# Performance work log

Hardware: AMD Instinct MI355X
Metric: run time of the kernel (lower is better)

## Reference

```python
import jax, jax.numpy as jnp
import numpy as np
from jax import lax

B, C, H, W = 8, 128, 128, 128


def setup_inputs() -> dict:
    key = jax.random.key(0)
    ks = jax.random.split(key, 10)
    s = 0.02
    return {
        "x": jax.random.normal(ks[0], (B, C, H, W), jnp.float32),
        "ln_w": jnp.ones((C,), jnp.float32),
        "ln_b": jnp.zeros((C,), jnp.float32),
        "qkv_w": jax.random.normal(ks[1], (3 * C, C, 1, 1), jnp.float32) * s,
        "qkv_b": jnp.zeros((3 * C,), jnp.float32),
        "dw_w": jax.random.normal(ks[2], (3 * C, 1, 3, 3), jnp.float32) * s,
        "dw_b": jnp.zeros((3 * C,), jnp.float32),
        "proj_w": jax.random.normal(ks[3], (C, C, 1, 1), jnp.float32) * s,
        "proj_b": jnp.zeros((C,), jnp.float32),
        "temp1": jnp.ones((1, 1), jnp.float32),
        "temp2": jnp.ones((1, 1), jnp.float32),
    }


def reference(x, ln_w, ln_b, qkv_w, qkv_b, dw_w, dw_b, proj_w, proj_b, temp1, temp2):
    Cd = x.shape[1]

    def ln(t):  # WithBias LayerNorm over channel dim (unbiased=False var)
        mu = t.mean(axis=1, keepdims=True)
        var = ((t - mu) ** 2).mean(axis=1, keepdims=True)
        return (t - mu) / jnp.sqrt(var + 1e-5) * ln_w[None, :, None, None] + ln_b[None, :, None, None]

    def conv1(t, w, b):  # 1x1 conv
        return jnp.einsum('bchw,oc->bohw', t, w[:, :, 0, 0]) + b[None, :, None, None]

    def dwc(t):  # depthwise 3x3, pad 1
        y = lax.conv_general_dilated(t, dw_w, (1, 1), ((1, 1), (1, 1)),
                                     dimension_numbers=('NCHW', 'OIHW', 'NCHW'),
                                     feature_group_count=t.shape[1])
        return y + dw_b[None, :, None, None]

    def l2n(t):  # F.normalize over last axis, eps=1e-12
        return t / jnp.maximum(jnp.linalg.norm(t, axis=-1, keepdims=True), 1e-12)

    # ---- stage 1: pool over H, attention over W (channel-pooled) ----
    qkv = dwc(conv1(ln(x), qkv_w, qkv_b))
    q1, k1, v1 = qkv[:, :Cd], qkv[:, Cd:2 * Cd], qkv[:, 2 * Cd:]
    q1 = l2n(q1.mean(axis=2)[:, None])           # [B,1,C,W]
    k1 = l2n(k1.max(axis=2)[:, None])            # [B,1,C,W]
    attn1 = jax.nn.softmax(jnp.einsum('bocw,bocv->bowv', q1, k1) * temp1, axis=-1)  # [B,1,W,W]
    out1 = jnp.einsum('bchw,bowv->bchv', v1, attn1)
    out1 = x + conv1(out1, proj_w, proj_b)

    # ---- stage 2: pool over C, attention over H ----
    qkv = dwc(conv1(ln(out1), qkv_w, qkv_b))
    q2, k2, v2 = qkv[:, :Cd], qkv[:, Cd:2 * Cd], qkv[:, 2 * Cd:]
    q2 = l2n(q2.mean(axis=1)[:, None])           # [B,1,H,W]
    k2 = l2n(k2.mean(axis=1)[:, None])           # [B,1,H,W]
    attn2 = jax.nn.softmax(jnp.einsum('bohw,bogw->bohg', q2, k2) * temp2, axis=-1)  # [B,1,H,H]
    out2 = jnp.einsum('bchw,bohg->bcgw', v2, attn2)  # = (v^T @ attn)^T
    out = conv1(out2, proj_w, proj_b) + out1
    return out
```

## Files before the change

### kernel.cpp

```cpp
#include <hip/hip_runtime.h>

typedef __attribute__((ext_vector_type(8))) short bf16x8;
typedef __attribute__((ext_vector_type(4))) float f32x4;
typedef __attribute__((ext_vector_type(4))) unsigned short us4;
typedef __attribute__((ext_vector_type(4))) unsigned int u32x4;

static constexpr int CC = 128, NN = 16384;
static constexpr int O3 = 384;
static constexpr long long CN  = (long long)CC * NN;
static constexpr long long O3N = (long long)O3 * NN;

__device__ __forceinline__ float wave_sum(float v) {
  for (int o = 32; o; o >>= 1) v += __shfl_xor(v, o);
  return v;
}
__device__ __forceinline__ float wave_max(float v) {
  for (int o = 32; o; o >>= 1) v = fmaxf(v, __shfl_xor(v, o));
  return v;
}
__device__ __forceinline__ unsigned short f2bf(float f) {
  unsigned u = __float_as_uint(f);
  u += 0x7FFF + ((u >> 16) & 1);
  return (unsigned short)(u >> 16);
}
__device__ __forceinline__ float bf2f(unsigned short h) {
  return __uint_as_float((unsigned)h << 16);
}

__global__ __launch_bounds__(64) void k_prep(const float* __restrict__ qkvw,
                                             const float* __restrict__ qkvb,
                                             const float* __restrict__ lnw,
                                             const float* __restrict__ lnb,
                                             const float* __restrict__ projw,
                                             unsigned short* __restrict__ Aq,
                                             unsigned short* __restrict__ Ap,
                                             float* __restrict__ Svec,
                                             float* __restrict__ bias2) {
  int o = blockIdx.x, t = threadIdx.x;
  if (o < O3) {
    float w0 = qkvw[o * 128 + t], w1 = qkvw[o * 128 + t + 64];
    unsigned short h0 = f2bf(w0 * lnw[t]), h1 = f2bf(w1 * lnw[t + 64]);
    Aq[o * 128 + t] = h0; Aq[o * 128 + t + 64] = h1;
    float s = wave_sum(bf2f(h0) + bf2f(h1));
    float bs = wave_sum(w0 * lnb[t] + w1 * lnb[t + 64]);
    if (t == 0) { Svec[o] = s; bias2[o] = qkvb[o] + bs; }
  } else {
    int r = o - O3;
    Ap[r * 128 + t] = f2bf(projw[r * 128 + t]);
    Ap[r * 128 + t + 64] = f2bf(projw[r * 128 + t + 64]);
  }
}

__global__ __launch_bounds__(256) void k_qkv_mfma(
    const float* __restrict__ x, const float* __restrict__ mu, const float* __restrict__ rs,
    const unsigned short* __restrict__ Aq, const float* __restrict__ Svec,
    const float* __restrict__ bias2, unsigned short* __restrict__ out, int b0, int useg) {
  __shared__ unsigned short As[128 * 136];
  __shared__ unsigned short Bs[64 * 128];
  __shared__ float muL[64], rsL[64];
  int bz = blockIdx.z, bg = b0 + bz;
  int p = blockIdx.x;
  int hi = p / 24, rr0 = p - hi * 24;
  int m0 = (rr0 >> 3) * 128;
  int n0 = (hi * 8 + (rr0 & 7)) * 64;
  int t = threadIdx.x, w = t >> 6, l = t & 63;
  int lr = l & 15, lg = l >> 4;
  const float* xb = x + (size_t)bg * CN + n0;

  {
    const unsigned short* Asrc = Aq + (size_t)m0 * 128;
#pragma unroll
    for (int r = 0; r < 8; ++r) {
      int v = r * 256 + t;
      int m = v >> 4, c8 = (v & 15) * 8;
      *(u32x4*)&As[m * 136 + c8] = *(const u32x4*)&Asrc[m * 128 + c8];
    }
  }
  {
    int n = t & 63, cb = t >> 6;
    float xr[32];
#pragma unroll
    for (int g = 0; g < 4; ++g)
#pragma unroll
      for (int q = 0; q < 8; ++q)
        xr[g * 8 + q] = xb[(size_t)((cb * 4 + g) * 8 + q) * NN + n];
#pragma unroll
    for (int g = 0; g < 4; ++g) {
      int c8 = (cb * 4 + g) * 8;
      unsigned pk[4];
#pragma unroll
      for (int q = 0; q < 4; ++q) {
        unsigned short a = f2bf(xr[g * 8 + 2 * q]);
        unsigned short b = f2bf(xr[g * 8 + 2 * q + 1]);
        pk[q] = (unsigned)a | ((unsigned)b << 16);
      }
      int c8s = c8 ^ ((n & 7) << 3);
      *(u32x4*)&Bs[n * 128 + c8s] = *(const u32x4*)pk;
    }
  }
  __syncthreads();

  if (!useg) {
    int pp = t >> 2, sub = t & 3;
    float s1 = 0.f, s2 = 0.f;
#pragma unroll
    for (int b2 = 0; b2 < 4; ++b2) {
      int c8 = (sub * 4 + b2) * 8;
      int c8s = c8 ^ ((pp & 7) << 3);
      bf16x8 v = *(const bf16x8*)&Bs[pp * 128 + c8s];
#pragma unroll
      for (int q = 0; q < 8; ++q) {
        float f = bf2f((unsigned short)v[q]);
        s1 += f; s2 += f * f;
      }
    }
    s1 += __shfl_xor(s1, 1); s2 += __shfl_xor(s2, 1);
    s1 += __shfl_xor(s1, 2); s2 += __shfl_xor(s2, 2);
    if (sub == 0) {
      float m = s1 * (1.f / 128.f);
      muL[pp] = m;
      rsL[pp] = rsqrtf(s2 * (1.f / 128.f) - m * m + 1e-5f);
    }
  }
  __syncthreads();

  f32x4 acc[2][4];
#pragma unroll
  for (int i = 0; i < 2; ++i)
#pragma unroll
    for (int j = 0; j < 4; ++j) acc[i][j] = (f32x4){0.f, 0.f, 0.f, 0.f};
#pragma unroll
  for (int ks = 0; ks < 4; ++ks) {
    bf16x8 bfr[4];
#pragma unroll
    for (int j = 0; j < 4; ++j) {
      int row = 16 * j + lr;
      int col = (ks * 32 + lg * 8) ^ ((lr & 7) << 3);
      bfr[j] = *(const bf16x8*)&Bs[row * 128 + col];
    }
#pragma unroll
    for (int i = 0; i < 2; ++i) {
      bf16x8 afr = *(const bf16x8*)&As[(32 * w + 16 * i + lr) * 136 + ks * 32 + lg * 8];
#pragma unroll
      for (int j = 0; j < 4; ++j)
        acc[i][j] = __builtin_amdgcn_mfma_f32_16x16x32_bf16(afr, bfr[j], acc[i][j], 0, 0, 0);
    }
  }

  float rsv[4], muv[4];
#pragma unroll
  for (int j = 0; j < 4; ++j) {
    int nl = 16 * j + lr;
    if (useg) {
      rsv[j] = rs[(size_t)bg * NN + n0 + nl];
      muv[j] = mu[(size_t)bg * NN + n0 + nl];
    } else {
      rsv[j] = rsL[nl];
      muv[j] = muL[nl];
    }
  }
#pragma unroll
  for (int i = 0; i < 2; ++i) {
    int ob = m0 + 32 * w + 16 * i + lg * 4;
    float sv[4], bv[4];
#pragma unroll
    for (int r2 = 0; r2 < 4; ++r2) { sv[r2] = Svec[ob + r2]; bv[r2] = bias2[ob + r2]; }
#pragma unroll
    for (int j = 0; j < 4; ++j) {
      int n = n0 + 16 * j + lr;
      unsigned short* op = out + (size_t)bz * O3N + n;
#pragma unroll
      for (int r2 = 0; r2 < 4; ++r2)
        op[(size_t)(ob + r2) * NN] = f2bf(rsv[j] * (acc[i][j][r2] - muv[j] * sv[r2]) + bv[r2]);
    }
  }
}

__global__ __launch_bounds__(1024) void k_dwc(unsigned short* __restrict__ buf,
                                              const float* __restrict__ dww,
                                              const float* __restrict__ dwb,
                                              float* __restrict__ qm,
                                              float* __restrict__ km,
                                              int b0, int stage) {
  __shared__ unsigned short pl[130 * 144];
  __shared__ float red[32 * 128];
  int o = blockIdx.x, bz = blockIdx.y, bg = b0 + bz;
  int t = threadIdx.x;
  unsigned short* base = buf + (size_t)bz * O3N + (size_t)o * NN;
  unsigned* pl32 = (unsigned*)pl;

  for (int i = t; i < 1168; i += 1024) {
    int idx;
    if (i < 72) idx = i;
    else if (i < 144) idx = 129 * 72 + (i - 72);
    else { int j = i - 144; int row = (j >> 3) + 1; int s = j & 7;
           idx = row * 72 + (s < 4 ? s : 64 + s); }
    pl32[idx] = 0u;
  }
  __syncthreads();
#pragma unroll
  for (int r = 0; r < 2; ++r) {
    int idx = r * 1024 + t;
    int row = idx >> 4, c8 = (idx & 15) * 8;
    *(u32x4*)&pl[(row + 1) * 144 + 8 + c8] = *(const u32x4*)&base[row * 128 + c8];
  }
  __syncthreads();

  const float* wg = dww + o * 9;
  float w00 = wg[0], w01 = wg[1], w02 = wg[2];
  float w10 = wg[3], w11 = wg[4], w12 = wg[5];
  float w20 = wg[6], w21 = wg[7], w22 = wg[8];
  float bias = dwb[o];
  int mode = (stage == 0) ? (o < 128 ? 1 : (o < 256 ? 2 : 0)) : 0;
  int hh0 = t >> 5, w0 = (t & 31) * 4;
  float csum[4] = {0.f, 0.f, 0.f, 0.f};
  float cmax[4] = {-1e30f, -1e30f, -1e30f, -1e30f};

#pragma unroll
  for (int g = 0; g < 4; ++g) {
    int h = g * 32 + hh0;
    float a0 = bias, a1 = bias, a2 = bias, a3 = bias;
#pragma unroll
    for (int dr = 0; dr < 3; ++dr) {
      const unsigned short* rp = &pl[(h + dr) * 144];
      us4 cA = *(const us4*)&rp[w0 + 4];
      us4 cB = *(const us4*)&rp[w0 + 8];
      us4 cC = *(const us4*)&rp[w0 + 12];
      float f0 = bf2f(cA[3]), f1 = bf2f(cB[0]), f2 = bf2f(cB[1]);
      float f3 = bf2f(cB[2]), f4 = bf2f(cB[3]), f5 = bf2f(cC[0]);
      float wr0 = (dr == 0) ? w00 : (dr == 1 ? w10 : w20);
      float wr1 = (dr == 0) ? w01 : (dr == 1 ? w11 : w21);
      float wr2 = (dr == 0) ? w02 : (dr == 1 ? w12 : w22);
      a0 += f0 * wr0 + f1 * wr1 + f2 * wr2;
      a1 += f1 * wr0 + f2 * wr1 + f3 * wr2;
      a2 += f2 * wr0 + f3 * wr1 + f4 * wr2;
      a3 += f3 * wr0 + f4 * wr1 + f5 * wr2;
    }
    if (mode == 0) {
      us4 ov;
      ov[0] = f2bf(a0); ov[1] = f2bf(a1); ov[2] = f2bf(a2); ov[3] = f2bf(a3);
      *(us4*)&base[g * 4096 + t * 4] = ov;
    } else if (mode == 1) {
      csum[0] += a0; csum[1] += a1; csum[2] += a2; csum[3] += a3;
    } else {
      cmax[0] = fmaxf(cmax[0], a0); cmax[1] = fmaxf(cmax[1], a1);
      cmax[2] = fmaxf(cmax[2], a2); cmax[3] = fmaxf(cmax[3], a3);
    }
  }

  if (mode) {
    int j = t >> 5;
#pragma unroll
    for (int dx = 0; dx < 4; ++dx)
      red[j * 128 + w0 + dx] = (mode == 1) ? csum[dx] : cmax[dx];
    __syncthreads();
    if (t < 128) {
      float v = red[t];
      if (mode == 1) {
        for (int jj = 1; jj < 32; ++jj) v += red[jj * 128 + t];
        qm[(size_t)bg * NN + o * 128 + t] = v * (1.f / 128.f);
      } else {
        for (int jj = 1; jj < 32; ++jj) v = fmaxf(v, red[jj * 128 + t]);
        km[(size_t)bg * NN + (o - 128) * 128 + t] = v;
      }
    }
  }
}

__global__ __launch_bounds__(256) void k_reduce2(const unsigned short* __restrict__ qkv,
                                                 float* __restrict__ qm, float* __restrict__ km,
                                                 int b0) {
  int bz = blockIdx.y;
  int n = blockIdx.x * 256 + threadIdx.x;
  const unsigned short* base = qkv + (size_t)bz * O3N + n;
  float sq = 0.f, sk = 0.f;
#pragma unroll 4
  for (int c = 0; c < 128; ++c) {
    sq += bf2f(base[(size_t)c * NN]);
    sk += bf2f(base[(size_t)(c + 128) * NN]);
  }
  size_t off = (size_t)(b0 + bz) * NN + n;
  qm[off] = sq * (1.f / 128.f);
  km[off] = sk * (1.f / 128.f);
}

__global__ void k_norm2(float* __restrict__ qm, float* __restrict__ km, int row0) {
  float* buf = blockIdx.y ? km : qm;
  int r = row0 + blockIdx.x, t = threadIdx.x;
  float* p = buf + (size_t)r * 128;
  float v0 = p[t], v1 = p[t + 64];
  float s = wave_sum(v0 * v0 + v1 * v1);
  float sc = 1.f / fmaxf(sqrtf(s), 1e-12f);
  p[t] = v0 * sc;
  p[t + 64] = v1 * sc;
}

__global__ void k_attn1(const float* __restrict__ qm, const float* __restrict__ km,
                        const float* __restrict__ temp, unsigned short* __restrict__ attnT,
                        int b0) {
  int bg = b0 + blockIdx.y;
  int i = blockIdx.x, t = threadIdx.x;
  const float* qb = qm + (size_t)bg * NN;
  const float* kb = km + (size_t)bg * NN;
  __shared__ float qcol[128];
  __shared__ float wred[2];
  qcol[t] = qb[t * 128 + i];
  __syncthreads();
  float s = 0.f;
#pragma unroll 4
  for (int k = 0; k < 128; ++k) s += qcol[k] * kb[k * 128 + t];
  s *= temp[0];
  int wid = t >> 6, lane = t & 63;
  float mx = wave_max(s);
  if (lane == 0) wred[wid] = mx;
  __syncthreads();
  mx = fmaxf(wred[0], wred[1]);
  float pv = __expf(s - mx);
  __syncthreads();
  float sm = wave_sum(pv);
  if (lane == 0) wred[wid] = sm;
  __syncthreads();
  float denom = wred[0] + wred[1];
  attnT[(size_t)bg * NN + (size_t)t * 128 + i] = f2bf(pv / denom);
}

__global__ void k_attn2(const float* __restrict__ qm, const float* __restrict__ km,
                        const float* __restrict__ temp, unsigned short* __restrict__ attnT,
                        int b0) {
  int bg = b0 + blockIdx.y;
  int i = blockIdx.x, t = threadIdx.x;
  const float* qb = qm + (size_t)bg * NN + i * 128;
  const float* kb = km + (size_t)bg * NN + (size_t)t * 128;
  __shared__ float qrow[128];
  __shared__ float wred[2];
  qrow[t] = qb[t];
  __syncthreads();
  float s = 0.f;
#pragma unroll 4
  for (int w = 0; w < 128; ++w) s += qrow[w] * kb[w];
  s *= temp[0];
  int wid = t >> 6, lane = t & 63;
  float mx = wave_max(s);
  if (lane == 0) wred[wid] = mx;
  __syncthreads();
  mx = fmaxf(wred[0], wred[1]);
  float pv = __expf(s - mx);
  __syncthreads();
  float sm = wave_sum(pv);
  if (lane == 0) wred[wid] = sm;
  __syncthreads();
  float denom = wred[0] + wred[1];
  attnT[(size_t)bg * NN + (size_t)t * 128 + i] = f2bf(pv / denom);
}

__global__ __launch_bounds__(256) void k_apply1_mfma(unsigned short* __restrict__ buf,
                                                     const unsigned short* __restrict__ attnT,
                                                     int b0) {
  __shared__ unsigned short Al[128 * 136];
  __shared__ unsigned short Bl[128 * 136];
  int bz = blockIdx.z, bg = b0 + bz;
  int m0 = blockIdx.x * 128;
  int t = threadIdx.x, w = t >> 6, l = t & 63, lr = l & 15, lg = l >> 4;
  const unsigned short* asrc = buf + (size_t)bz * O3N + (size_t)256 * NN + (size_t)m0 * 128;
  const unsigned short* bsrc = attnT + (size_t)bg * NN;
#pragma unroll
  for (int r = 0; r < 8; ++r) {
    int idx = r * 256 + t;
    int row = idx >> 4, c8 = (idx & 15) * 8;
    *(u32x4*)&Al[row * 136 + c8] = *(const u32x4*)&asrc[row * 128 + c8];
    *(u32x4*)&Bl[row * 136 + c8] = *(const u32x4*)&bsrc[row * 128 + c8];
  }
  __syncthreads();
  f32x4 acc[2][8];
#pragma unroll
  for (int i = 0; i < 2; ++i)
#pragma unroll
    for (int j = 0; j < 8; ++j) acc[i][j] = (f32x4){0.f, 0.f, 0.f, 0.f};
#pragma unroll
  for (int ks = 0; ks < 4; ++ks) {
    bf16x8 bfr[8];
#pragma unroll
    for (int j = 0; j < 8; ++j)
      bfr[j] = *(const bf16x8*)&Bl[(16 * j + lr) * 136 + ks * 32 + lg * 8];
#pragma unroll
    for (int i = 0; i < 2; ++i) {
      bf16x8 afr = *(const bf16x8*)&Al[(32 * w + 16 * i + lr) * 136 + ks * 32 + lg * 8];
#pragma unroll
      for (int j = 0; j < 8; ++j)
        acc[i][j] = __builtin_amdgcn_mfma_f32_16x16x32_bf16(afr, bfr[j], acc[i][j], 0, 0, 0);
    }
  }
  unsigned short* ob = buf + (size_t)bz * O3N;
#pragma unroll
  for (int i = 0; i < 2; ++i)
#pragma unroll
    for (int j = 0; j < 8; ++j)
#pragma unroll
      for (int r2 = 0; r2 < 4; ++r2) {
        int m = m0 + 32 * w + 16 * i + lg * 4 + r2;
        int n = 16 * j + lr;
        ob[(size_t)m * 128 + n] = f2bf(acc[i][j][r2]);
      }
}

__global__ __launch_bounds__(256) void k_apply2_mfma(unsigned short* __restrict__ buf,
                                                     const unsigned short* __restrict__ attnT,
                                                     int b0) {
  __shared__ unsigned short At[128 * 136];
  __shared__ unsigned short Bt[128 * 136];
  int bz = blockIdx.z, bg = b0 + bz, c = blockIdx.x;
  int t = threadIdx.x, w = t >> 6, l = t & 63, lr = l & 15, lg = l >> 4;
  const unsigned short* vsrc = buf + (size_t)bz * O3N + (size_t)(256 + c) * NN;
  const unsigned short* asrc = attnT + (size_t)bg * NN;
#pragma unroll
  for (int r = 0; r < 8; ++r) {
    int idx = r * 256 + t;
    int row = idx >> 4, c8 = (idx & 15) * 8;
    *(u32x4*)&At[row * 136 + c8] = *(const u32x4*)&asrc[row * 128 + c8];
    us4 lo = *(const us4*)&vsrc[row * 128 + c8];
    us4 hi = *(const us4*)&vsrc[row * 128 + c8 + 4];
#pragma unroll
    for (int q = 0; q < 4; ++q) {
      Bt[(c8 + q) * 136 + row] = lo[q];
      Bt[(c8 + 4 + q) * 136 + row] = hi[q];
    }
  }
  __syncthreads();
  f32x4 acc[2][8];
#pragma unroll
  for (int i = 0; i < 2; ++i)
#pragma unroll
    for (int j = 0; j < 8; ++j) acc[i][j] = (f32x4){0.f, 0.f, 0.f, 0.f};
#pragma unroll
  for (int ks = 0; ks < 4; ++ks) {
    bf16x8 bfr[8];
#pragma unroll
    for (int j = 0; j < 8; ++j)
      bfr[j] = *(const bf16x8*)&Bt[(16 * j + lr) * 136 + ks * 32 + lg * 8];
#pragma unroll
    for (int i = 0; i < 2; ++i) {
      bf16x8 afr = *(const bf16x8*)&At[(32 * w + 16 * i + lr) * 136 + ks * 32 + lg * 8];
#pragma unroll
      for (int j = 0; j < 8; ++j)
        acc[i][j] = __builtin_amdgcn_mfma_f32_16x16x32_bf16(afr, bfr[j], acc[i][j], 0, 0, 0);
    }
  }
  unsigned short* ob = buf + (size_t)bz * O3N + (size_t)c * NN;
#pragma unroll
  for (int i = 0; i < 2; ++i)
#pragma unroll
    for (int j = 0; j < 8; ++j)
#pragma unroll
      for (int r2 = 0; r2 < 4; ++r2) {
        int g = 32 * w + 16 * i + lg * 4 + r2;
        int n = 16 * j + lr;
        ob[(size_t)g * 128 + n] = f2bf(acc[i][j][r2]);
      }
}

__global__ __launch_bounds__(256) void k_proj_mfma(
    const unsigned short* __restrict__ tin, const unsigned short* __restrict__ Ap,
    const float* __restrict__ pb, const float* __restrict__ res,
    float* __restrict__ dst, float* __restrict__ mu, float* __restrict__ rs,
    int b0, int do_stats) {
  __shared__ unsigned short Al[128 * 136];
  __shared__ unsigned short Bs2[64 * 128];
  __shared__ float red1[64 * 17];
  __shared__ float red2[64 * 17];
  int bz = blockIdx.z, bg = b0 + bz;
  int n0 = blockIdx.x * 64;
  int t = threadIdx.x, w = t >> 6, l = t & 63, lr = l & 15, lg = l >> 4;
  const unsigned short* tb = tin + (size_t)bz * O3N + n0;

#pragma unroll
  for (int r = 0; r < 8; ++r) {
    int v = r * 256 + t;
    int m = v >> 4, c8 = (v & 15) * 8;
    *(u32x4*)&Al[m * 136 + c8] = *(const u32x4*)&Ap[m * 128 + c8];
  }
  {
    int n = t & 63, cb = t >> 6;
    unsigned short vr[32];
#pragma unroll
    for (int g = 0; g < 4; ++g)
#pragma unroll
      for (int q = 0; q < 8; ++q)
        vr[g * 8 + q] = tb[(size_t)((cb * 4 + g) * 8 + q) * NN + n];
#pragma unroll
    for (int g = 0; g < 4; ++g) {
      int c8 = (cb * 4 + g) * 8;
      unsigned pk[4];
#pragma unroll
      for (int q = 0; q < 4; ++q)
        pk[q] = (unsigned)vr[g * 8 + 2 * q] | ((unsigned)vr[g * 8 + 2 * q + 1] << 16);
      int c8s = c8 ^ ((n & 7) << 3);
      *(u32x4*)&Bs2[n * 128 + c8s] = *(const u32x4*)pk;
    }
  }
  __syncthreads();

  f32x4 acc[2][4];
#pragma unroll
  for (int i = 0; i < 2; ++i)
#pragma unroll
    for (int j = 0; j < 4; ++j) acc[i][j] = (f32x4){0.f, 0.f, 0.f, 0.f};

#pragma unroll
  for (int ks = 0; ks < 4; ++ks) {
    bf16x8 bfr[4];
#pragma unroll
    for (int j = 0; j < 4; ++j) {
      int row = 16 * j + lr;
      int col = (ks * 32 + lg * 8) ^ ((lr & 7) << 3);
      bfr[j] = *(const bf16x8*)&Bs2[row * 128 + col];
    }
#pragma unroll
    for (int i = 0; i < 2; ++i) {
      bf16x8 afr = *(const bf16x8*)&Al[(32 * w + 16 * i + lr) * 136 + ks * 32 + lg * 8];
#pragma unroll
      for (int j = 0; j < 4; ++j)
        acc[i][j] = __builtin_amdgcn_mfma_f32_16x16x32_bf16(afr, bfr[j], acc[i][j], 0, 0, 0);
    }
  }

  float s1p[4] = {0.f, 0.f, 0.f, 0.f}, s2p[4] = {0.f, 0.f, 0.f, 0.f};
#pragma unroll
  for (int i = 0; i < 2; ++i) {
    int ob = 32 * w + 16 * i + lg * 4;
    float bv[4];
#pragma unroll
    for (int r2 = 0; r2 < 4; ++r2) bv[r2] = pb[ob + r2];
#pragma unroll
    for (int j = 0; j < 4; ++j) {
      int n = n0 + 16 * j + lr;
#pragma unroll
      for (int r2 = 0; r2 < 4; ++r2) {
        size_t off = (size_t)bg * CN + (size_t)(ob + r2) * NN + n;
        float val = acc[i][j][r2] + bv[r2] + res[off];
        dst[off] = val;
        s1p[j] += val;
        s2p[j] += val * val;
      }
    }
  }
  if (do_stats) {
#pragma unroll
    for (int j = 0; j < 4; ++j) {
      red1[(16 * j + lr) * 17 + (w * 4 + lg)] = s1p[j];
      red2[(16 * j + lr) * 17 + (w * 4 + lg)] = s2p[j];
    }
    __syncthreads();
    if (t < 64) {
      float s1 = 0.f, s2 = 0.f;
#pragma unroll
      for (int kk = 0; kk < 16; ++kk) { s1 += red1[t * 17 + kk]; s2 += red2[t * 17 + kk]; }
      float m = s1 * (1.f / 128.f);
      float var = s2 * (1.f / 128.f) - m * m;
      mu[(size_t)bg * NN + n0 + t] = m;
      rs[(size_t)bg * NN + n0 + t] = rsqrtf(var + 1e-5f);
    }
  }
}

extern "C" void kernel_launch(void* const* d_in, const int* in_sizes, int n_in,
                              void* d_out, int out_size, void* d_ws, size_t ws_size,
                              hipStream_t stream) {
  (void)in_sizes; (void)n_in; (void)out_size;
  const float* x     = (const float*)d_in[0];
  const float* lnw   = (const float*)d_in[1];
  const float* lnb   = (const float*)d_in[2];
  const float* qkvw  = (const float*)d_in[3];
  const float* qkvb  = (const float*)d_in[4];
  const float* dww   = (const float*)d_in[5];
  const float* dwb   = (const float*)d_in[6];
  const float* projw = (const float*)d_in[7];
  const float* projb = (const float*)d_in[8];
  const float* temp1 = (const float*)d_in[9];
  const float* temp2 = (const float*)d_in[10];
  float* out = (float*)d_out;
  float* ws = (float*)d_ws;

  auto needBytes = [&](int nb) {
    return ((size_t)nb * (O3N / 2) + 4ull * 131072 + 65536 + 768 + 24576 + 8192) * 4;
  };
  int NB = 8;
  while (NB > 1 && ws_size < needBytes(NB)) NB >>= 1;
  if (ws_size < needBytes(1)) return;

  unsigned short* convbuf = (unsigned short*)ws;
  float* mu = ws + (size_t)NB * (O3N / 2);
  float* rs = mu + 131072;
  float* qm = rs + 131072;
  float* km = qm + 131072;
  unsigned short* attnT = (unsigned short*)(km + 131072);
  float* Svec  = (float*)(attnT + 8ull * NN);
  float* bias2 = Svec + 384;
  unsigned short* Aq = (unsigned short*)(bias2 + 384);
  unsigned short* Ap = Aq + 49152;

  k_prep<<<512, 64, 0, stream>>>(qkvw, qkvb, lnw, lnb, projw, Aq, Ap, Svec, bias2);

  for (int stage = 0; stage < 2; ++stage) {
    const float* src = stage ? out : x;
    for (int b0 = 0; b0 < 8; b0 += NB) {
      k_qkv_mfma<<<dim3(768, 1, NB), 256, 0, stream>>>(src, mu, rs, Aq, Svec, bias2, convbuf,
                                                       b0, stage);
      k_dwc<<<dim3(384, NB), 1024, 0, stream>>>(convbuf, dww, dwb, qm, km, b0, stage);
      if (stage == 1)
        k_reduce2<<<dim3(64, NB), 256, 0, stream>>>(convbuf, qm, km, b0);
      k_norm2<<<dim3(NB * 128, 2), 64, 0, stream>>>(qm, km, b0 * 128);
      if (stage == 0)
        k_attn1<<<dim3(128, NB), 128, 0, stream>>>(qm, km, temp1, attnT, b0);
      else
        k_attn2<<<dim3(128, NB), 128, 0, stream>>>(qm, km, temp2, attnT, b0);
      if (stage == 0)
        k_apply1_mfma<<<dim3(128, 1, NB), 256, 0, stream>>>(convbuf, attnT, b0);
      else
        k_apply2_mfma<<<dim3(128, 1, NB), 256, 0, stream>>>(convbuf, attnT, b0);
      const float* resp = stage ? out : x;
      k_proj_mfma<<<dim3(256, 1, NB), 256, 0, stream>>>(convbuf, Ap, projb, resp, out,
                                                        mu, rs, b0, stage == 0 ? 1 : 0);
    }
  }
}
```

Measured before the change: 296.6 us.

## Fuse stage-1 attention apply with projection and store intermediate in bf16

Stage-1 attention application, 1x1 projection, residual add and LayerNorm statistics now run in one kernel per row h, so the attention output no longer goes through the conv buffer in global memory. The stage-1 result is kept as a bf16 buffer rather than fp32. Stage 2 reads that buffer directly into the QKV GEMM and as the final residual. This cuts global traffic and a launch, but adds bf16 rounding on the residual path and uses more workspace.

```diff
diff --git a/kernel.cpp b/kernel.cpp
--- a/kernel.cpp
+++ b/kernel.cpp
@@ -52,9 +52,10 @@
 }
 
 __global__ __launch_bounds__(256) void k_qkv_mfma(
-    const float* __restrict__ x, const float* __restrict__ mu, const float* __restrict__ rs,
+    const void* __restrict__ srcp, const float* __restrict__ mu, const float* __restrict__ rs,
     const unsigned short* __restrict__ Aq, const float* __restrict__ Svec,
-    const float* __restrict__ bias2, unsigned short* __restrict__ out, int b0, int useg) {
+    const float* __restrict__ bias2, unsigned short* __restrict__ out,
+    int b0, int useg, int srcbf) {
   __shared__ unsigned short As[128 * 136];
   __shared__ unsigned short Bs[64 * 128];
   __shared__ float muL[64], rsL[64];
@@ -65,7 +66,6 @@
   int n0 = (hi * 8 + (rr0 & 7)) * 64;
   int t = threadIdx.x, w = t >> 6, l = t & 63;
   int lr = l & 15, lg = l >> 4;
-  const float* xb = x + (size_t)bg * CN + n0;
 
   {
     const unsigned short* Asrc = Aq + (size_t)m0 * 128;
@@ -78,24 +78,45 @@
   }
   {
     int n = t & 63, cb = t >> 6;
-    float xr[32];
-#pragma unroll
-    for (int g = 0; g < 4; ++g)
-#pragma unroll
-      for (int q = 0; q < 8; ++q)
-        xr[g * 8 + q] = xb[(size_t)((cb * 4 + g) * 8 + q) * NN + n];
-#pragma unroll
-    for (int g = 0; g < 4; ++g) {
-      int c8 = (cb * 4 + g) * 8;
-      unsigned pk[4];
-#pragma unroll
-      for (int q = 0; q < 4; ++q) {
-        unsigned short a = f2bf(xr[g * 8 + 2 * q]);
-        unsigned short b = f2bf(xr[g * 8 + 2 * q + 1]);
-        pk[q] = (unsigned)a | ((unsigned)b << 16);
+    if (!srcbf) {
+      const float* xb = (const float*)srcp + (size_t)bg * CN + n0;
+      float xr[32];
+#pragma unroll
+      for (int g = 0; g < 4; ++g)
+#pragma unroll
+        for (int q = 0; q < 8; ++q)
+          xr[g * 8 + q] = xb[(size_t)((cb * 4 + g) * 8 + q) * NN + n];
+#pragma unroll
+      for (int g = 0; g < 4; ++g) {
+        int c8 = (cb * 4 + g) * 8;
+        unsigned pk[4];
+#pragma unroll
+        for (int q = 0; q < 4; ++q) {
+          unsigned short a = f2bf(xr[g * 8 + 2 * q]);
+          unsigned short b = f2bf(xr[g * 8 + 2 * q + 1]);
+          pk[q] = (unsigned)a | ((unsigned)b << 16);
+        }
+        int c8s = c8 ^ ((n & 7) << 3);
+        *(u32x4*)&Bs[n * 128 + c8s] = *(const u32x4*)pk;
       }
-      int c8s = c8 ^ ((n & 7) << 3);
-      *(u32x4*)&Bs[n * 128 + c8s] = *(const u32x4*)pk;
+    } else {
+      const unsigned short* xb = (const unsigned short*)srcp + (size_t)bg * CN + n0;
+      unsigned short xr[32];
+#pragma unroll
+      for (int g = 0; g < 4; ++g)
+#pragma unroll
+        for (int q = 0; q < 8; ++q)
+          xr[g * 8 + q] = xb[(size_t)((cb * 4 + g) * 8 + q) * NN + n];
+#pragma unroll
+      for (int g = 0; g < 4; ++g) {
+        int c8 = (cb * 4 + g) * 8;
+        unsigned pk[4];
+#pragma unroll
+        for (int q = 0; q < 4; ++q)
+          pk[q] = (unsigned)xr[g * 8 + 2 * q] | ((unsigned)xr[g * 8 + 2 * q + 1] << 16);
+        int c8s = c8 ^ ((n & 7) << 3);
+        *(u32x4*)&Bs[n * 128 + c8s] = *(const u32x4*)pk;
+      }
     }
   }
   __syncthreads();
@@ -121,8 +142,8 @@
       muL[pp] = m;
       rsL[pp] = rsqrtf(s2 * (1.f / 128.f) - m * m + 1e-5f);
     }
-  }
-  __syncthreads();
+    __syncthreads();
+  }
 
   f32x4 acc[2][4];
 #pragma unroll
@@ -353,54 +374,136 @@
   attnT[(size_t)bg * NN + (size_t)t * 128 + i] = f2bf(pv / denom);
 }
 
-__global__ __launch_bounds__(256) void k_apply1_mfma(unsigned short* __restrict__ buf,
-                                                     const unsigned short* __restrict__ attnT,
-                                                     int b0) {
-  __shared__ unsigned short Al[128 * 136];
-  __shared__ unsigned short Bl[128 * 136];
-  int bz = blockIdx.z, bg = b0 + bz;
-  int m0 = blockIdx.x * 128;
-  int t = threadIdx.x, w = t >> 6, l = t & 63, lr = l & 15, lg = l >> 4;
-  const unsigned short* asrc = buf + (size_t)bz * O3N + (size_t)256 * NN + (size_t)m0 * 128;
-  const unsigned short* bsrc = attnT + (size_t)bg * NN;
+__global__ __launch_bounds__(256) void k_ap1(const unsigned short* __restrict__ buf,
+                                             const unsigned short* __restrict__ attnT,
+                                             const unsigned short* __restrict__ Ap,
+                                             const float* __restrict__ pb,
+                                             const float* __restrict__ x,
+                                             unsigned short* __restrict__ out1,
+                                             float* __restrict__ mu, float* __restrict__ rs,
+                                             int b0) {
+  __shared__ __attribute__((aligned(16))) unsigned short S[32768];
+  unsigned short* TA = S;
+  unsigned short* TB = S + 16384;
+  int h = blockIdx.x, bz = blockIdx.z, bg = b0 + bz;
+  int t = threadIdx.x, wv = t >> 6, l = t & 63, lr = l & 15, lg = l >> 4;
+
+  {
+    const unsigned short* vbase = buf + (size_t)bz * O3N + (size_t)256 * NN;
+    const unsigned short* abase = attnT + (size_t)bg * NN;
+#pragma unroll
+    for (int r = 0; r < 8; ++r) {
+      int idx = r * 256 + t;
+      int row = idx >> 4, c8 = (idx & 15) * 8;
+      int c8s = c8 ^ ((row & 7) << 3);
+      *(u32x4*)&TA[row * 128 + c8s] = *(const u32x4*)&vbase[((size_t)row * 128 + h) * 128 + c8];
+      *(u32x4*)&TB[row * 128 + c8s] = *(const u32x4*)&abase[row * 128 + c8];
+    }
+  }
+  __syncthreads();
+
+  f32x4 acc[2][8];
+#pragma unroll
+  for (int i = 0; i < 2; ++i)
+#pragma unroll
+    for (int j = 0; j < 8; ++j) acc[i][j] = (f32x4){0.f, 0.f, 0.f, 0.f};
+#pragma unroll
+  for (int ks = 0; ks < 4; ++ks) {
+    int colx = (ks * 32 + lg * 8) ^ ((lr & 7) << 3);
+    bf16x8 bfr[8];
+#pragma unroll
+    for (int j = 0; j < 8; ++j)
+      bfr[j] = *(const bf16x8*)&TB[(16 * j + lr) * 128 + colx];
+#pragma unroll
+    for (int i = 0; i < 2; ++i) {
+      bf16x8 afr = *(const bf16x8*)&TA[(32 * wv + 16 * i + lr) * 128 + colx];
+#pragma unroll
+      for (int j = 0; j < 8; ++j)
+        acc[i][j] = __builtin_amdgcn_mfma_f32_16x16x32_bf16(afr, bfr[j], acc[i][j], 0, 0, 0);
+    }
+  }
+  __syncthreads();
+
+#pragma unroll
+  for (int i = 0; i < 2; ++i) {
+    int c0 = 32 * wv + 16 * i + lg * 4;
+#pragma unroll
+    for (int j = 0; j < 8; ++j) {
+      int v = 16 * j + lr;
+      us4 ov;
+#pragma unroll
+      for (int r2 = 0; r2 < 4; ++r2) ov[r2] = f2bf(acc[i][j][r2]);
+      *(us4*)&TA[v * 128 + (c0 ^ ((v & 7) << 3))] = ov;
+    }
+  }
 #pragma unroll
   for (int r = 0; r < 8; ++r) {
     int idx = r * 256 + t;
     int row = idx >> 4, c8 = (idx & 15) * 8;
-    *(u32x4*)&Al[row * 136 + c8] = *(const u32x4*)&asrc[row * 128 + c8];
-    *(u32x4*)&Bl[row * 136 + c8] = *(const u32x4*)&bsrc[row * 128 + c8];
-  }
-  __syncthreads();
-  f32x4 acc[2][8];
+    *(u32x4*)&TB[row * 128 + (c8 ^ ((row & 7) << 3))] = *(const u32x4*)&Ap[row * 128 + c8];
+  }
+  __syncthreads();
+
 #pragma unroll
   for (int i = 0; i < 2; ++i)
 #pragma unroll
     for (int j = 0; j < 8; ++j) acc[i][j] = (f32x4){0.f, 0.f, 0.f, 0.f};
 #pragma unroll
   for (int ks = 0; ks < 4; ++ks) {
+    int colx = (ks * 32 + lg * 8) ^ ((lr & 7) << 3);
     bf16x8 bfr[8];
 #pragma unroll
     for (int j = 0; j < 8; ++j)
-      bfr[j] = *(const bf16x8*)&Bl[(16 * j + lr) * 136 + ks * 32 + lg * 8];
+      bfr[j] = *(const bf16x8*)&TA[(16 * j + lr) * 128 + colx];
 #pragma unroll
     for (int i = 0; i < 2; ++i) {
-      bf16x8 afr = *(const bf16x8*)&Al[(32 * w + 16 * i + lr) * 136 + ks * 32 + lg * 8];
+      bf16x8 afr = *(const bf16x8*)&TB[(32 * wv + 16 * i + lr) * 128 + colx];
 #pragma unroll
       for (int j = 0; j < 8; ++j)
         acc[i][j] = __builtin_amdgcn_mfma_f32_16x16x32_bf16(afr, bfr[j], acc[i][j], 0, 0, 0);
     }
   }
-  unsigned short* ob = buf + (size_t)bz * O3N;
-#pragma unroll
-  for (int i = 0; i < 2; ++i)
-#pragma unroll
-    for (int j = 0; j < 8; ++j)
+
+  float s1p[8], s2p[8];
+#pragma unroll
+  for (int j = 0; j < 8; ++j) { s1p[j] = 0.f; s2p[j] = 0.f; }
+#pragma unroll
+  for (int i = 0; i < 2; ++i) {
+    int o0 = 32 * wv + 16 * i + lg * 4;
+    float bv[4];
+#pragma unroll
+    for (int r2 = 0; r2 < 4; ++r2) bv[r2] = pb[o0 + r2];
+#pragma unroll
+    for (int j = 0; j < 8; ++j) {
+      int n = h * 128 + 16 * j + lr;
 #pragma unroll
       for (int r2 = 0; r2 < 4; ++r2) {
-        int m = m0 + 32 * w + 16 * i + lg * 4 + r2;
-        int n = 16 * j + lr;
-        ob[(size_t)m * 128 + n] = f2bf(acc[i][j][r2]);
+        size_t off = (size_t)bg * CN + (size_t)(o0 + r2) * NN + n;
+        float val = acc[i][j][r2] + bv[r2] + x[off];
+        out1[off] = f2bf(val);
+        s1p[j] += val;
+        s2p[j] += val * val;
       }
+    }
+  }
+  __syncthreads();
+  float* red1 = (float*)S;
+  float* red2 = red1 + 128 * 17;
+#pragma unroll
+  for (int j = 0; j < 8; ++j) {
+    red1[(16 * j + lr) * 17 + (wv * 4 + lg)] = s1p[j];
+    red2[(16 * j + lr) * 17 + (wv * 4 + lg)] = s2p[j];
+  }
+  __syncthreads();
+  if (t < 128) {
+    float s1 = 0.f, s2 = 0.f;
+#pragma unroll
+    for (int kk = 0; kk < 16; ++kk) { s1 += red1[t * 17 + kk]; s2 += red2[t * 17 + kk]; }
+    float m = s1 * (1.f / 128.f);
+    float var = s2 * (1.f / 128.f) - m * m;
+    mu[(size_t)bg * NN + h * 128 + t] = m;
+    rs[(size_t)bg * NN + h * 128 + t] = rsqrtf(var + 1e-5f);
+  }
 }
 
 __global__ __launch_bounds__(256) void k_apply2_mfma(unsigned short* __restrict__ buf,
@@ -460,13 +563,10 @@
 
 __global__ __launch_bounds__(256) void k_proj_mfma(
     const unsigned short* __restrict__ tin, const unsigned short* __restrict__ Ap,
-    const float* __restrict__ pb, const float* __restrict__ res,
-    float* __restrict__ dst, float* __restrict__ mu, float* __restrict__ rs,
-    int b0, int do_stats) {
+    const float* __restrict__ pb, const unsigned short* __restrict__ res,
+    float* __restrict__ dst, int b0) {
   __shared__ unsigned short Al[128 * 136];
   __shared__ unsigned short Bs2[64 * 128];
-  __shared__ float red1[64 * 17];
-  __shared__ float red2[64 * 17];
   int bz = blockIdx.z, bg = b0 + bz;
   int n0 = blockIdx.x * 64;
   int t = threadIdx.x, w = t >> 6, l = t & 63, lr = l & 15, lg = l >> 4;
@@ -523,7 +623,6 @@
     }
   }
 
-  float s1p[4] = {0.f, 0.f, 0.f, 0.f}, s2p[4] = {0.f, 0.f, 0.f, 0.f};
 #pragma unroll
   for (int i = 0; i < 2; ++i) {
     int ob = 32 * w + 16 * i + lg * 4;
@@ -536,28 +635,8 @@
 #pragma unroll
       for (int r2 = 0; r2 < 4; ++r2) {
         size_t off = (size_t)bg * CN + (size_t)(ob + r2) * NN + n;
-        float val = acc[i][j][r2] + bv[r2] + res[off];
-        dst[off] = val;
-        s1p[j] += val;
-        s2p[j] += val * val;
+        dst[off] = acc[i][j][r2] + bv[r2] + bf2f(res[off]);
       }
-    }
-  }
-  if (do_stats) {
-#pragma unroll
-    for (int j = 0; j < 4; ++j) {
-      red1[(16 * j + lr) * 17 + (w * 4 + lg)] = s1p[j];
-      red2[(16 * j + lr) * 17 + (w * 4 + lg)] = s2p[j];
-    }
-    __syncthreads();
-    if (t < 64) {
-      float s1 = 0.f, s2 = 0.f;
-#pragma unroll
-      for (int kk = 0; kk < 16; ++kk) { s1 += red1[t * 17 + kk]; s2 += red2[t * 17 + kk]; }
-      float m = s1 * (1.f / 128.f);
-      float var = s2 * (1.f / 128.f) - m * m;
-      mu[(size_t)bg * NN + n0 + t] = m;
-      rs[(size_t)bg * NN + n0 + t] = rsqrtf(var + 1e-5f);
     }
   }
 }
@@ -581,14 +660,15 @@
   float* ws = (float*)d_ws;
 
   auto needBytes = [&](int nb) {
-    return ((size_t)nb * (O3N / 2) + 4ull * 131072 + 65536 + 768 + 24576 + 8192) * 4;
+    return ((size_t)nb * (O3N / 2) + 4ull * CN + 4ull * 131072 + 65536 + 768 + 24576 + 8192) * 4;
   };
   int NB = 8;
   while (NB > 1 && ws_size < needBytes(NB)) NB >>= 1;
   if (ws_size < needBytes(1)) return;
 
   unsigned short* convbuf = (unsigned short*)ws;
-  float* mu = ws + (size_t)NB * (O3N / 2);
+  unsigned short* out1 = (unsigned short*)(ws + (size_t)NB * (O3N / 2));
+  float* mu = ws + (size_t)NB * (O3N / 2) + 4ull * CN;
   float* rs = mu + 131072;
   float* qm = rs + 131072;
   float* km = qm + 131072;
@@ -600,26 +680,22 @@
 
   k_prep<<<512, 64, 0, stream>>>(qkvw, qkvb, lnw, lnb, projw, Aq, Ap, Svec, bias2);
 
-  for (int stage = 0; stage < 2; ++stage) {
-    const float* src = stage ? out : x;
-    for (int b0 = 0; b0 < 8; b0 += NB) {
-      k_qkv_mfma<<<dim3(768, 1, NB), 256, 0, stream>>>(src, mu, rs, Aq, Svec, bias2, convbuf,
-                                                       b0, stage);
-      k_dwc<<<dim3(384, NB), 1024, 0, stream>>>(convbuf, dww, dwb, qm, km, b0, stage);
-      if (stage == 1)
-        k_reduce2<<<dim3(64, NB), 256, 0, stream>>>(convbuf, qm, km, b0);
-      k_norm2<<<dim3(NB * 128, 2), 64, 0, stream>>>(qm, km, b0 * 128);
-      if (stage == 0)
-        k_attn1<<<dim3(128, NB), 128, 0, stream>>>(qm, km, temp1, attnT, b0);
-      else
-        k_attn2<<<dim3(128, NB), 128, 0, stream>>>(qm, km, temp2, attnT, b0);
-      if (stage == 0)
-        k_apply1_mfma<<<dim3(128, 1, NB), 256, 0, stream>>>(convbuf, attnT, b0);
-      else
-        k_apply2_mfma<<<dim3(128, 1, NB), 256, 0, stream>>>(convbuf, attnT, b0);
-      const float* resp = stage ? out : x;
-      k_proj_mfma<<<dim3(256, 1, NB), 256, 0, stream>>>(convbuf, Ap, projb, resp, out,
-                                                        mu, rs, b0, stage == 0 ? 1 : 0);
-    }
-  }
-}
+  for (int b0 = 0; b0 < 8; b0 += NB) {
+    k_qkv_mfma<<<dim3(768, 1, NB), 256, 0, stream>>>(x, mu, rs, Aq, Svec, bias2, convbuf,
+                                                     b0, 0, 0);
+    k_dwc<<<dim3(384, NB), 1024, 0, stream>>>(convbuf, dww, dwb, qm, km, b0, 0);
+    k_norm2<<<dim3(NB * 128, 2), 64, 0, stream>>>(qm, km, b0 * 128);
+    k_attn1<<<dim3(128, NB), 128, 0, stream>>>(qm, km, temp1, attnT, b0);
+    k_ap1<<<dim3(128, 1, NB), 256, 0, stream>>>(convbuf, attnT, Ap, projb, x, out1, mu, rs, b0);
+  }
+  for (int b0 = 0; b0 < 8; b0 += NB) {
+    k_qkv_mfma<<<dim3(768, 1, NB), 256, 0, stream>>>(out1, mu, rs, Aq, Svec, bias2, convbuf,
+                                                     b0, 1, 1);
+    k_dwc<<<dim3(384, NB), 1024, 0, stream>>>(convbuf, dww, dwb, qm, km, b0, 1);
+    k_reduce2<<<dim3(64, NB), 256, 0, stream>>>(convbuf, qm, km, b0);
+    k_norm2<<<dim3(NB * 128, 2), 64, 0, stream>>>(qm, km, b0 * 128);
+    k_attn2<<<dim3(128, NB), 128, 0, stream>>>(qm, km, temp2, attnT, b0);
+    k_apply2_mfma<<<dim3(128, 1, NB), 256, 0, stream>>>(convbuf, attnT, b0);
+    k_proj_mfma<<<dim3(256, 1, NB), 256, 0, stream>>>(convbuf, Ap, projb, out1, out, b0);
+  }
+}
```

After: 274.7 us, median of 2. 7.4% less time.
